# Kernel optimization log

Hardware: AMD Instinct MI355X
Metric: run time of the kernel (lower is better)

## Reference

```python
import jax, jax.numpy as jnp
import numpy as np

SCORE_SCALE = 1.0
Z_LOSS_COEF = 0.001
LB_LOSS_COEF = 0.01
N_EXPERTS = 64
TOP_K = 2
D_MODEL = 4096
T = 8192


def setup_inputs() -> dict:
    key = jax.random.key(0)
    kx, kw = jax.random.split(key)
    x = jax.random.normal(kx, (T, D_MODEL), dtype=jnp.float32)
    W = jax.random.normal(kw, (N_EXPERTS, D_MODEL), dtype=jnp.float32) * (1.0 / np.sqrt(D_MODEL))
    return {"x": x, "W": W}


def reference(x, W):
    # router logits: [T, E]
    logits = jnp.einsum('td,ed->te', x, W) * SCORE_SCALE
    probs = jax.nn.softmax(logits, axis=-1)
    # top-k gating
    topk_scores, topk_experts = jax.lax.top_k(probs, TOP_K)  # [T,k], [T,k]
    denom = jnp.clip(jnp.sum(topk_scores, axis=-1, keepdims=True), 1e-9, None)
    topk_scores = topk_scores / denom
    # z-loss: mean of squared logsumexp
    z_loss = jnp.mean(jax.nn.logsumexp(logits, axis=-1) ** 2)
    # load-balance loss
    importance = jnp.sum(probs, axis=0)  # [E]
    top1 = topk_experts[:, 0]
    load = jax.ops.segment_sum(jnp.ones_like(top1, dtype=jnp.float32), top1,
                               num_segments=N_EXPERTS)  # bincount
    importance = importance / jnp.clip(jnp.sum(importance), 1e-9, None)
    load = load / jnp.clip(jnp.sum(load), 1e-9, None)
    lb_loss = jnp.sum(importance * load) * (N_EXPERTS ** 2)
    router_z_loss = z_loss * Z_LOSS_COEF
    load_balance_loss = lb_loss * LB_LOSS_COEF
    logits_mean = jax.lax.stop_gradient(jnp.mean(logits))
    return (topk_experts, topk_scores, router_z_loss, load_balance_loss, logits_mean)
```

## Files before the change

### kernel.cpp

```cpp
#include <hip/hip_runtime.h>
#include <math.h>


#define NT 8192
#define ND 4096
#define NE 64
#define W_OFF 512
#define WL_OFF (W_OFF + 131072)
#define SLAB2 (W_OFF + 262144)
#define BKD 64
#define SLAB_OFF 512

typedef float f32x4 __attribute__((ext_vector_type(4)));
typedef short s16x8 __attribute__((ext_vector_type(8)));

__device__ __forceinline__ void gload16(const float* g, float* l) {
    __builtin_amdgcn_global_load_lds(
        (const __attribute__((address_space(1))) void*)g,
        (__attribute__((address_space(3))) void*)l, 16, 0, 0);
}

__global__ __launch_bounds__(256)
void convert_w(const float* __restrict__ W, float* __restrict__ ws)
{
    if (blockIdx.x == 0 && threadIdx.x < 131) ws[threadIdx.x] = 0.f;

    const int s = blockIdx.x * 256 + threadIdx.x;
    const int sg  = s >> 8;
    const int nt  = (s >> 6) & 3;
    const int kb  = (s >> 4) & 3;
    const int e15 = s & 15;
    const int e   = nt * 16 + e15;
    const int k0  = sg * 32 + kb * 8;
    const float* wr = W + (size_t)e * ND + k0;

    union { s16x8 v; ushort u[8]; } h, l;
    #pragma unroll
    for (int j = 0; j < 8; j++) {
        const float v = wr[j];
        const unsigned ub = __float_as_uint(v);
        h.u[j] = (ushort)(ub >> 16);
        const float lo = v - __uint_as_float(ub & 0xffff0000u);
        l.u[j] = (ushort)(__float_as_uint(lo) >> 16);
    }
    *(s16x8*)((ushort*)(ws + W_OFF) + (size_t)s * 8) = h.v;
    *(s16x8*)((ushort*)(ws + WL_OFF) + (size_t)s * 8) = l.v;
}

#define CMFMA(va, vb, bh0, bh1, bl0, bl1)                                    \
    {                                                                        \
        union { s16x8 v; ushort u[8]; } ah, al;                              \
        _Pragma("unroll")                                                    \
        for (int i = 0; i < 4; i++) {                                        \
            const unsigned u0 = __float_as_uint(va[i]);                      \
            ah.u[i] = (ushort)(u0 >> 16);                                    \
            const float l0 = va[i] - __uint_as_float(u0 & 0xffff0000u);      \
            al.u[i] = (ushort)(__float_as_uint(l0) >> 16);                   \
            const unsigned u1 = __float_as_uint(vb[i]);                      \
            ah.u[4 + i] = (ushort)(u1 >> 16);                                \
            const float l1 = vb[i] - __uint_as_float(u1 & 0xffff0000u);      \
            al.u[4 + i] = (ushort)(__float_as_uint(l1) >> 16);               \
        }                                                                    \
        acc0 = __builtin_amdgcn_mfma_f32_16x16x32_bf16(ah.v, bh0, acc0, 0,0,0);\
        acc1 = __builtin_amdgcn_mfma_f32_16x16x32_bf16(ah.v, bh1, acc1, 0,0,0);\
        acc0 = __builtin_amdgcn_mfma_f32_16x16x32_bf16(al.v, bh0, acc0, 0,0,0);\
        acc1 = __builtin_amdgcn_mfma_f32_16x16x32_bf16(al.v, bh1, acc1, 0,0,0);\
        acc0 = __builtin_amdgcn_mfma_f32_16x16x32_bf16(ah.v, bl0, acc0, 0,0,0);\
        acc1 = __builtin_amdgcn_mfma_f32_16x16x32_bf16(ah.v, bl1, acc1, 0,0,0);\
    }

__global__ __launch_bounds__(512, 2)
void pass1_lds(const float* __restrict__ x, float* __restrict__ ws)
{
    __shared__ float  xbuf[2][4096];
    __shared__ ushort wbuf[2][8192];

    const int tid  = threadIdx.x;
    const int wv   = tid >> 6, lane = tid & 63;
    const int mt   = wv >> 1,  ng   = wv & 1;
    const int bq   = blockIdx.x >> 7;
    const int tb   = blockIdx.x & 127;
    const int tok0 = tb * 64;
    const int ntg0 = ng * 2, ntg1 = ng * 2 + 1;
    const int k0   = bq << 10;

    const int t0 = tid >> 4, j0 = tid & 15;
    const int t1 = t0 + 32;
    const float* xg0 = x + (size_t)(tok0 + t0) * ND + k0 + ((j0 ^ (t0 & 7)) << 2);
    const float* xg1 = x + (size_t)(tok0 + t1) * ND + k0 + ((j0 ^ (t1 & 7)) << 2);
    const ushort* whg = (const ushort*)(ws + W_OFF);
    const ushort* wlg = (const ushort*)(ws + WL_OFF);

#define STAGE(bb, cc)                                                        \
    {                                                                        \
        gload16(xg0 + (cc) * 64, &xbuf[bb][tid * 4]);                        \
        gload16(xg1 + (cc) * 64, &xbuf[bb][2048 + tid * 4]);                 \
        const size_t cb = ((size_t)(bq * 32 + (cc) * 2) * 4096)              \
                        + (size_t)tid * 16;                                  \
        gload16((const float*)((const char*)whg + cb),                       \
                (float*)&wbuf[bb][(size_t)tid * 8]);                         \
        gload16((const float*)((const char*)wlg + cb),                       \
                (float*)&wbuf[bb][4096 + (size_t)tid * 8]);                  \
    }

    f32x4 acc0 = {0.f, 0.f, 0.f, 0.f};
    f32x4 acc1 = {0.f, 0.f, 0.f, 0.f};

    const int tl  = mt * 16 + (lane & 15);
    const int swz = lane & 7;
    const int kb4 = (lane >> 4) * 2;

    STAGE(0, 0);
    __syncthreads();

    int b = 0;
    #pragma unroll 1
    for (int c = 0; c < 16; ++c) {
        if (c + 1 < 16) STAGE(b ^ 1, c + 1);
        const char*   xb = (const char*)xbuf[b] + tl * 256;
        const ushort* wb = wbuf[b];
        #pragma unroll
        for (int ks = 0; ks < 2; ++ks) {
            const f32x4 va = *(const f32x4*)(xb + (((ks * 8 + kb4)     ^ swz) << 4));
            const f32x4 vb = *(const f32x4*)(xb + (((ks * 8 + kb4 + 1) ^ swz) << 4));
            const s16x8 bh0 = *(const s16x8*)(wb + ((ks * 4 + ntg0) << 9) + lane * 8);
            const s16x8 bh1 = *(const s16x8*)(wb + ((ks * 4 + ntg1) << 9) + lane * 8);
            const s16x8 bl0 = *(const s16x8*)(wb + 4096 + ((ks * 4 + ntg0) << 9) + lane * 8);
            const s16x8 bl1 = *(const s16x8*)(wb + 4096 + ((ks * 4 + ntg1) << 9) + lane * 8);
            CMFMA(va, vb, bh0, bh1, bl0, bl1);
        }
        __syncthreads();
        b ^= 1;
    }
#undef STAGE

    float* slab = ws + SLAB2 + (size_t)bq * NT * NE;
    const int er = (lane >> 4) * 4;
    #pragma unroll
    for (int r = 0; r < 4; r++) {
        const int token = tok0 + mt * 16 + er + r;
        slab[(size_t)token * NE + ntg0 * 16 + (lane & 15)] = acc0[r];
        slab[(size_t)token * NE + ntg1 * 16 + (lane & 15)] = acc1[r];
    }
}

#define LOADX(dst, off)                                                      \
    {                                                                        \
        _Pragma("unroll")                                                    \
        for (int t = 0; t < 8; t++)                                          \
            dst[t] = *reinterpret_cast<const float4*>(                       \
                xp + (size_t)t * ND + (off));                                \
    }
#define COMP(xv, wptr, wstride)                                              \
    {                                                                        \
        float4 wvv[8];                                                       \
        _Pragma("unroll")                                                    \
        for (int e = 0; e < 8; e++)                                          \
            wvv[e] = *reinterpret_cast<const float4*>((wptr) + e * (wstride));\
        _Pragma("unroll")                                                    \
        for (int e = 0; e < 8; e++) {                                        \
            _Pragma("unroll")                                                \
            for (int t = 0; t < 8; t++) {                                    \
                float a = acc[t][e];                                         \
                a = fmaf(xv[t].x, wvv[e].x, a);                              \
                a = fmaf(xv[t].y, wvv[e].y, a);                              \
                a = fmaf(xv[t].z, wvv[e].z, a);                              \
                a = fmaf(xv[t].w, wvv[e].w, a);                              \
                acc[t][e] = a;                                               \
            }                                                                \
        }                                                                    \
    }

__global__ __launch_bounds__(256, 2)
void pass1_dbuf(const float* __restrict__ x, const float* __restrict__ W,
                float* __restrict__ ws, int kq_bits, int nchunk)
{
    __shared__ float wbuf[2][NE * BKD];
    const int tid  = threadIdx.x;
    const int wave = tid >> 6;
    const int lane = tid & 63;
    const int eg   = lane >> 3;
    const int ks   = lane & 7;
    const int bq   = blockIdx.x >> 8;
    const int tb   = blockIdx.x & 255;
    const int tok0 = tb * 32 + wave * 8;
    const int k0   = bq * (ND >> kq_bits);

    float acc[8][8];
    #pragma unroll
    for (int t = 0; t < 8; t++)
        #pragma unroll
        for (int e = 0; e < 8; e++) acc[t][e] = 0.f;

    const float* xp = x + (size_t)tok0 * ND + k0 + ks * 4;
    #pragma unroll
    for (int r = 0; r < 4; r++) {
        int s = r * 256 + tid;
        gload16(W + (size_t)(s >> 4) * ND + k0 + (s & 15) * 4, &wbuf[0][s << 2]);
    }
    float4 xa[8], xb[8];
    LOADX(xa, 0);
    __syncthreads();

    #pragma unroll 1
    for (int c = 0; c < nchunk; ++c) {
        const int b = c & 1;
        if (c + 1 < nchunk) {
            const int koff = k0 + (c + 1) * BKD;
            #pragma unroll
            for (int r = 0; r < 4; r++) {
                int s = r * 256 + tid;
                gload16(W + (size_t)(s >> 4) * ND + koff + (s & 15) * 4,
                        &wbuf[b ^ 1][s << 2]);
            }
        }
        LOADX(xb, c * BKD + 32);
        COMP(xa, &wbuf[b][(eg * 8) * BKD + ks * 4], BKD);
        if (c + 1 < nchunk) LOADX(xa, (c + 1) * BKD);
        COMP(xb, &wbuf[b][(eg * 8) * BKD + 32 + ks * 4], BKD);
        __syncthreads();
    }

    #pragma unroll
    for (int t = 0; t < 8; t++)
        #pragma unroll
        for (int e = 0; e < 8; e++) {
            float v = acc[t][e];
            v += __shfl_xor(v, 1);
            v += __shfl_xor(v, 2);
            v += __shfl_xor(v, 4);
            acc[t][e] = v;
        }
    float* slab = ws + SLAB_OFF + ((size_t)bq * NT + tok0) * NE;
    #pragma unroll
    for (int t = 0; t < 8; t++) {
        if (ks == t) {
            *reinterpret_cast<float4*>(slab + (size_t)t * NE + eg * 8) =
                make_float4(acc[t][0], acc[t][1], acc[t][2], acc[t][3]);
            *reinterpret_cast<float4*>(slab + (size_t)t * NE + eg * 8 + 4) =
                make_float4(acc[t][4], acc[t][5], acc[t][6], acc[t][7]);
        }
    }
}

__global__ __launch_bounds__(128)
void pass2(float* __restrict__ ws, float* __restrict__ out, int kq,
           int slab_base, int nblocks, int do_fuse)
{
    __shared__ float imp_s[NE];
    __shared__ float load_s[NE];
    __shared__ int lastflag;
    const int tid  = threadIdx.x;
    const int lane = tid & 63;
    if (tid < NE) { imp_s[tid] = 0.f; load_s[tid] = 0.f; }
    __syncthreads();

    const int tok = blockIdx.x * 128 + tid;
    float lgv[NE];
    {
        const float* p0 = ws + slab_base + (size_t)tok * NE;
        #pragma unroll
        for (int e4 = 0; e4 < 16; e4++) {
            float4 v = *reinterpret_cast<const float4*>(p0 + e4 * 4);
            lgv[e4*4+0] = v.x; lgv[e4*4+1] = v.y;
            lgv[e4*4+2] = v.z; lgv[e4*4+3] = v.w;
        }
        for (int q = 1; q < kq; q++) {
            const float* pq = ws + slab_base + ((size_t)q * NT + tok) * NE;
            #pragma unroll
            for (int e4 = 0; e4 < 16; e4++) {
                float4 v = *reinterpret_cast<const float4*>(pq + e4 * 4);
                lgv[e4*4+0] += v.x; lgv[e4*4+1] += v.y;
                lgv[e4*4+2] += v.z; lgv[e4*4+3] += v.w;
            }
        }
    }

    float m = -3.0e38f;
    #pragma unroll
    for (int e = 0; e < NE; e++) m = fmaxf(m, lgv[e]);
    float se = 0.f, ssum = 0.f;
    #pragma unroll
    for (int e = 0; e < NE; e++) { ssum += lgv[e]; se += __expf(lgv[e] - m); }
    const float lse = m + __logf(se);
    const float inv = 1.f / se;

    #pragma unroll
    for (int e = 0; e < NE; e++) lgv[e] = __expf(lgv[e] - m) * inv;

    float v1 = -3.0e38f, v2 = -3.0e38f;
    int   i1 = 0, i2 = 0;
    #pragma unroll
    for (int e = 0; e < NE; e++) {
        const float v = lgv[e];
        if (v > v1)      { v2 = v1; i2 = i1; v1 = v; i1 = e; }
        else if (v > v2) { v2 = v;  i2 = e; }
    }
    const float dn = fmaxf(v1 + v2, 1e-9f);

    out[2 * tok]              = (float)i1;
    out[2 * tok + 1]          = (float)i2;
    out[2 * NT + 2 * tok]     = v1 / dn;
    out[2 * NT + 2 * tok + 1] = v2 / dn;
    atomicAdd(&load_s[i1], 1.0f);

    float zv = lse * lse, sv = ssum;
    #pragma unroll
    for (int mk = 1; mk < 64; mk <<= 1) {
        zv += __shfl_xor(zv, mk);
        sv += __shfl_xor(sv, mk);
    }
    if (lane == 0) { atomicAdd(&ws[128], zv); atomicAdd(&ws[129], sv); }

    float impacc = 0.f;
    #pragma unroll
    for (int e = 0; e < NE; e++) {
        float v = lgv[e];
        #pragma unroll
        for (int mk = 1; mk < 64; mk <<= 1) v += __shfl_xor(v, mk);
        if (lane == e) impacc = v;
    }
    atomicAdd(&imp_s[lane], impacc);

    __syncthreads();
    if (tid < NE) {
        atomicAdd(&ws[tid], imp_s[tid]);
        atomicAdd(&ws[NE + tid], load_s[tid]);
    }

    if (!do_fuse) return;

    __threadfence();
    if (tid == 0) {
        const int old = atomicAdd((int*)(ws + 130), 1);
        lastflag = (old == nblocks - 1);
    }
    __syncthreads();
    if (lastflag && tid < 64) {
        const float imp = atomicAdd(&ws[tid], 0.f);
        const float ld  = atomicAdd(&ws[NE + tid], 0.f);
        float is = imp, ls = ld;
        #pragma unroll
        for (int mk = 1; mk < 64; mk <<= 1) {
            is += __shfl_xor(is, mk);
            ls += __shfl_xor(ls, mk);
        }
        float v = (imp / fmaxf(is, 1e-9f)) * (ld / fmaxf(ls, 1e-9f));
        #pragma unroll
        for (int mk = 1; mk < 64; mk <<= 1) v += __shfl_xor(v, mk);
        if (tid == 0) {
            const float zz = atomicAdd(&ws[128], 0.f);
            const float ss = atomicAdd(&ws[129], 0.f);
            out[4 * NT]     = (zz / (float)NT) * 0.001f;
            out[4 * NT + 1] = v * (float)(NE * NE) * 0.01f;
            out[4 * NT + 2] = ss / (float)((size_t)NT * NE);
        }
    }
}

__global__ void finalize(const float* __restrict__ ws, float* __restrict__ out)
{
    const int l = threadIdx.x;
    const float imp = ws[l];
    const float ld  = ws[NE + l];
    float is = imp, ls = ld;
    #pragma unroll
    for (int mk = 1; mk < 64; mk <<= 1) { is += __shfl_xor(is, mk); ls += __shfl_xor(ls, mk); }
    float v = (imp / fmaxf(is, 1e-9f)) * (ld / fmaxf(ls, 1e-9f));
    #pragma unroll
    for (int mk = 1; mk < 64; mk <<= 1) v += __shfl_xor(v, mk);
    if (l == 0) {
        out[4 * NT]     = (ws[128] / (float)NT) * 0.001f;
        out[4 * NT + 1] = v * (float)(NE * NE) * 0.01f;
        out[4 * NT + 2] = ws[129] / (float)((size_t)NT * NE);
    }
}

extern "C" void kernel_launch(void* const* d_in, const int* in_sizes, int n_in,
                              void* d_out, int out_size, void* d_ws, size_t ws_size,
                              hipStream_t stream) {
    const float* x = (const float*)d_in[0];
    const float* W = (const float*)d_in[1];
    float* out = (float*)d_out;
    float* ws  = (float*)d_ws;

    const size_t need4 = (size_t)(SLAB2 + 4ull * NT * NE) * 4;
    if (ws_size >= need4) {
        hipLaunchKernelGGL(convert_w, dim3(128), dim3(256), 0, stream, W, ws);
        hipLaunchKernelGGL(pass1_lds, dim3(4 * 128), dim3(512), 0, stream, x, ws);
        hipLaunchKernelGGL(pass2, dim3(NT / 128), dim3(128), 0, stream,
                           ws, out, 4, SLAB2, NT / 128, 1);
    } else {
        hipMemsetAsync(ws, 0, 131 * sizeof(float), stream);
        int kq_bits = 2;
        if (ws_size < (SLAB_OFF + 4ull * NT * NE) * 4) kq_bits = 1;
        if (ws_size < (SLAB_OFF + 2ull * NT * NE) * 4) kq_bits = 0;
        const int kq = 1 << kq_bits;
        const int nchunk = (ND >> kq_bits) / BKD;
        hipLaunchKernelGGL(pass1_dbuf, dim3(256 * kq), dim3(256), 0, stream,
                           x, W, ws, kq_bits, nchunk);
        hipLaunchKernelGGL(pass2, dim3(NT / 128), dim3(128), 0, stream,
                           ws, out, kq, SLAB_OFF, NT / 128, 0);
        hipLaunchKernelGGL(finalize, dim3(1), dim3(64), 0, stream, ws, out);
    }
}
```

Before: 52.55 us.

## Pre-split x tile into bf16 hi/lo in LDS, read W directly from global

```diff
diff --git a/kernel.cpp b/kernel.cpp
--- a/kernel.cpp
+++ b/kernel.cpp
@@ -13,6 +13,7 @@
 
 typedef float f32x4 __attribute__((ext_vector_type(4)));
 typedef short s16x8 __attribute__((ext_vector_type(8)));
+typedef short s16x4 __attribute__((ext_vector_type(4)));
 
 __device__ __forceinline__ void gload16(const float* g, float* l) {
     __builtin_amdgcn_global_load_lds(
@@ -47,100 +48,89 @@
     *(s16x8*)((ushort*)(ws + WL_OFF) + (size_t)s * 8) = l.v;
 }
 
-#define CMFMA(va, vb, bh0, bh1, bl0, bl1)                                    \
-    {                                                                        \
-        union { s16x8 v; ushort u[8]; } ah, al;                              \
-        _Pragma("unroll")                                                    \
-        for (int i = 0; i < 4; i++) {                                        \
-            const unsigned u0 = __float_as_uint(va[i]);                      \
-            ah.u[i] = (ushort)(u0 >> 16);                                    \
-            const float l0 = va[i] - __uint_as_float(u0 & 0xffff0000u);      \
-            al.u[i] = (ushort)(__float_as_uint(l0) >> 16);                   \
-            const unsigned u1 = __float_as_uint(vb[i]);                      \
-            ah.u[4 + i] = (ushort)(u1 >> 16);                                \
-            const float l1 = vb[i] - __uint_as_float(u1 & 0xffff0000u);      \
-            al.u[4 + i] = (ushort)(__float_as_uint(l1) >> 16);               \
-        }                                                                    \
-        acc0 = __builtin_amdgcn_mfma_f32_16x16x32_bf16(ah.v, bh0, acc0, 0,0,0);\
-        acc1 = __builtin_amdgcn_mfma_f32_16x16x32_bf16(ah.v, bh1, acc1, 0,0,0);\
-        acc0 = __builtin_amdgcn_mfma_f32_16x16x32_bf16(al.v, bh0, acc0, 0,0,0);\
-        acc1 = __builtin_amdgcn_mfma_f32_16x16x32_bf16(al.v, bh1, acc1, 0,0,0);\
-        acc0 = __builtin_amdgcn_mfma_f32_16x16x32_bf16(ah.v, bl0, acc0, 0,0,0);\
-        acc1 = __builtin_amdgcn_mfma_f32_16x16x32_bf16(ah.v, bl1, acc1, 0,0,0);\
-    }
-
 __global__ __launch_bounds__(512, 2)
-void pass1_lds(const float* __restrict__ x, float* __restrict__ ws)
-{
-    __shared__ float  xbuf[2][4096];
-    __shared__ ushort wbuf[2][8192];
+void pass1_ph(const float* __restrict__ x, float* __restrict__ ws)
+{
+    __shared__ ushort xh[16384];
+    __shared__ ushort xl[16384];
+    __shared__ float  red[4][64][4];
 
     const int tid  = threadIdx.x;
+    const int bq   = blockIdx.x >> 9;
+    const int tb   = blockIdx.x & 511;
+    const int tok0 = tb * 16;
+    const int k0   = bq << 10;
+
+    {
+        const int tok = tid >> 5;
+        const int s4  = tid & 31;
+        const float* xrow = x + (size_t)(tok0 + tok) * ND + k0;
+        f32x4 vx[8];
+        #pragma unroll
+        for (int j = 0; j < 8; j++)
+            vx[j] = *(const f32x4*)(xrow + s4 * 4 + j * 128);
+
+        const int kbw  = (s4 >> 1) & 3;
+        const int half = s4 & 1;
+        #pragma unroll
+        for (int j = 0; j < 8; j++) {
+            const int kstep = (s4 >> 3) + j * 4;
+            const int tokX  = tok ^ (kstep & 15);
+            const int base  = (kstep * 64 + kbw * 16 + tokX) * 8 + half * 4;
+            union { s16x4 v; ushort u[4]; } hh, ll;
+            #pragma unroll
+            for (int i = 0; i < 4; i++) {
+                const float v = vx[j][i];
+                const unsigned ub = __float_as_uint(v);
+                hh.u[i] = (ushort)(ub >> 16);
+                const float lo = v - __uint_as_float(ub & 0xffff0000u);
+                ll.u[i] = (ushort)(__float_as_uint(lo) >> 16);
+            }
+            *(s16x4*)(xh + base) = hh.v;
+            *(s16x4*)(xl + base) = ll.v;
+        }
+    }
+    __syncthreads();
+
     const int wv   = tid >> 6, lane = tid & 63;
-    const int mt   = wv >> 1,  ng   = wv & 1;
-    const int bq   = blockIdx.x >> 7;
-    const int tb   = blockIdx.x & 127;
-    const int tok0 = tb * 64;
-    const int ntg0 = ng * 2, ntg1 = ng * 2 + 1;
-    const int k0   = bq << 10;
-
-    const int t0 = tid >> 4, j0 = tid & 15;
-    const int t1 = t0 + 32;
-    const float* xg0 = x + (size_t)(tok0 + t0) * ND + k0 + ((j0 ^ (t0 & 7)) << 2);
-    const float* xg1 = x + (size_t)(tok0 + t1) * ND + k0 + ((j0 ^ (t1 & 7)) << 2);
-    const ushort* whg = (const ushort*)(ws + W_OFF);
-    const ushort* wlg = (const ushort*)(ws + WL_OFF);
-
-#define STAGE(bb, cc)                                                        \
-    {                                                                        \
-        gload16(xg0 + (cc) * 64, &xbuf[bb][tid * 4]);                        \
-        gload16(xg1 + (cc) * 64, &xbuf[bb][2048 + tid * 4]);                 \
-        const size_t cb = ((size_t)(bq * 32 + (cc) * 2) * 4096)              \
-                        + (size_t)tid * 16;                                  \
-        gload16((const float*)((const char*)whg + cb),                       \
-                (float*)&wbuf[bb][(size_t)tid * 8]);                         \
-        gload16((const float*)((const char*)wlg + cb),                       \
-                (float*)&wbuf[bb][4096 + (size_t)tid * 8]);                  \
-    }
+    const int nt   = wv & 3;
+    const int kh   = wv >> 2;
+    const int kb   = lane >> 4;
+    const int tokX0 = lane & 15;
+
+    const ushort* bb_h = (const ushort*)(ws + W_OFF)
+        + ((size_t)(bq * 32) * 256 + nt * 64 + kb * 16 + (lane & 15)) * 8;
+    const ushort* bb_l = (const ushort*)(ws + WL_OFF)
+        + ((size_t)(bq * 32) * 256 + nt * 64 + kb * 16 + (lane & 15)) * 8;
 
     f32x4 acc0 = {0.f, 0.f, 0.f, 0.f};
-    f32x4 acc1 = {0.f, 0.f, 0.f, 0.f};
-
-    const int tl  = mt * 16 + (lane & 15);
-    const int swz = lane & 7;
-    const int kb4 = (lane >> 4) * 2;
-
-    STAGE(0, 0);
-    __syncthreads();
-
-    int b = 0;
+
     #pragma unroll 1
-    for (int c = 0; c < 16; ++c) {
-        if (c + 1 < 16) STAGE(b ^ 1, c + 1);
-        const char*   xb = (const char*)xbuf[b] + tl * 256;
-        const ushort* wb = wbuf[b];
-        #pragma unroll
-        for (int ks = 0; ks < 2; ++ks) {
-            const f32x4 va = *(const f32x4*)(xb + (((ks * 8 + kb4)     ^ swz) << 4));
-            const f32x4 vb = *(const f32x4*)(xb + (((ks * 8 + kb4 + 1) ^ swz) << 4));
-            const s16x8 bh0 = *(const s16x8*)(wb + ((ks * 4 + ntg0) << 9) + lane * 8);
-            const s16x8 bh1 = *(const s16x8*)(wb + ((ks * 4 + ntg1) << 9) + lane * 8);
-            const s16x8 bl0 = *(const s16x8*)(wb + 4096 + ((ks * 4 + ntg0) << 9) + lane * 8);
-            const s16x8 bl1 = *(const s16x8*)(wb + 4096 + ((ks * 4 + ntg1) << 9) + lane * 8);
-            CMFMA(va, vb, bh0, bh1, bl0, bl1);
-        }
-        __syncthreads();
-        b ^= 1;
-    }
-#undef STAGE
-
-    float* slab = ws + SLAB2 + (size_t)bq * NT * NE;
-    const int er = (lane >> 4) * 4;
-    #pragma unroll
-    for (int r = 0; r < 4; r++) {
-        const int token = tok0 + mt * 16 + er + r;
-        slab[(size_t)token * NE + ntg0 * 16 + (lane & 15)] = acc0[r];
-        slab[(size_t)token * NE + ntg1 * 16 + (lane & 15)] = acc1[r];
+    for (int c = kh * 16; c < kh * 16 + 16; ++c) {
+        const int aidx = (c * 64 + kb * 16 + (tokX0 ^ (c & 15))) * 8;
+        const s16x8 ah = *(const s16x8*)(xh + aidx);
+        const s16x8 al = *(const s16x8*)(xl + aidx);
+        const s16x8 bh = *(const s16x8*)(bb_h + (size_t)c * 2048);
+        const s16x8 bl = *(const s16x8*)(bb_l + (size_t)c * 2048);
+        acc0 = __builtin_amdgcn_mfma_f32_16x16x32_bf16(ah, bh, acc0, 0, 0, 0);
+        acc0 = __builtin_amdgcn_mfma_f32_16x16x32_bf16(al, bh, acc0, 0, 0, 0);
+        acc0 = __builtin_amdgcn_mfma_f32_16x16x32_bf16(ah, bl, acc0, 0, 0, 0);
+    }
+
+    if (kh == 1) {
+        red[nt][lane][0] = acc0[0]; red[nt][lane][1] = acc0[1];
+        red[nt][lane][2] = acc0[2]; red[nt][lane][3] = acc0[3];
+    }
+    __syncthreads();
+    if (kh == 0) {
+        float* slab = ws + SLAB2 + (size_t)bq * NT * NE;
+        const int er = (lane >> 4) * 4;
+        #pragma unroll
+        for (int r = 0; r < 4; r++) {
+            const int token = tok0 + er + r;
+            slab[(size_t)token * NE + nt * 16 + (lane & 15)] =
+                acc0[r] + red[nt][lane][r];
+        }
     }
 }
 
@@ -387,7 +377,7 @@
     const size_t need4 = (size_t)(SLAB2 + 4ull * NT * NE) * 4;
     if (ws_size >= need4) {
         hipLaunchKernelGGL(convert_w, dim3(128), dim3(256), 0, stream, W, ws);
-        hipLaunchKernelGGL(pass1_lds, dim3(4 * 128), dim3(512), 0, stream, x, ws);
+        hipLaunchKernelGGL(pass1_ph, dim3(4 * 512), dim3(512), 0, stream, x, ws);
         hipLaunchKernelGGL(pass2, dim3(NT / 128), dim3(128), 0, stream,
                            ws, out, 4, SLAB2, NT / 128, 1);
     } else {
```

Measured after the change: 80.39 us. 53.0% more time.
